# Kernel tuning notes

Hardware: AMD Instinct MI355X
Metric: run time of the kernel (lower is better)

## Reference

```python
import jax, jax.numpy as jnp
import numpy as np

B, T, E = 2, 2048, 1024
H, D = 8, 512
ROPE_BASE = 10000.0


def apply_rope(x):
    # x: [B, H, T, D] -- rotary positional embedding, half-split convention
    t = x.shape[2]
    d = x.shape[3]
    inv_freq = 1.0 / (ROPE_BASE ** (jnp.arange(0, d, 2, dtype=jnp.float32) / d))  # [D/2]
    ang = jnp.arange(t, dtype=jnp.float32)[:, None] * inv_freq[None, :]           # [T, D/2]
    cos = jnp.cos(ang)[None, None].astype(x.dtype)
    sin = jnp.sin(ang)[None, None].astype(x.dtype)
    x1, x2 = jnp.split(x, 2, axis=-1)
    return jnp.concatenate([x1 * cos - x2 * sin, x1 * sin + x2 * cos], axis=-1)


def setup_inputs() -> dict:
    key = jax.random.key(0)
    ks = jax.random.split(key, 5)
    s_in = 1.0 / np.sqrt(E)
    s_out = 1.0 / np.sqrt(H * D)
    return {
        "x": jax.random.normal(ks[0], (B, T, E), dtype=jnp.float32),
        "Wq": jax.random.normal(ks[1], (H * D, E), dtype=jnp.float32) * s_in,
        "Wk": jax.random.normal(ks[2], (H * D, E), dtype=jnp.float32) * s_in,
        "Wv": jax.random.normal(ks[3], (H * D, E), dtype=jnp.float32) * s_in,
        "Wo": jax.random.normal(ks[4], (E, H * D), dtype=jnp.float32) * s_out,
    }


def reference(x, Wq, Wk, Wv, Wo):
    b, t, e = x.shape
    # QKV projections (bias-free Linear: x @ W.T), reshape to [B, H, T, D]
    q = (x @ Wq.T).reshape(b, t, H, D).transpose(0, 2, 1, 3)
    k = (x @ Wk.T).reshape(b, t, H, D).transpose(0, 2, 1, 3)
    v = (x @ Wv.T).reshape(b, t, H, D).transpose(0, 2, 1, 3)
    # RoPE on q and k
    q = apply_rope(q)
    k = apply_rope(k)
    # scaled dot-product attention with causal mask
    scale = 1.0 / jnp.sqrt(jnp.asarray(D, dtype=x.dtype))
    scores = jnp.einsum("bhqd,bhkd->bhqk", q, k) * scale
    causal = jnp.tril(jnp.ones((t, t), dtype=bool))
    scores = jnp.where(causal[None, None], scores, jnp.asarray(-jnp.inf, dtype=scores.dtype))
    probs = jax.nn.softmax(scores, axis=-1)  # explicitly materialized, as in source
    attn = jnp.einsum("bhqk,bhkd->bhqd", probs, v)
    out = attn.transpose(0, 2, 1, 3).reshape(b, t, H * D) @ Wo.T
    return out
```

## Files before the change

### kernel.cpp

```cpp
#include <hip/hip_runtime.h>


#define DEV __device__ __forceinline__

using bf16x8  = __attribute__((ext_vector_type(8))) short;
using floatx4 = __attribute__((ext_vector_type(4))) float;

#define MFMA16(a, b, c) __builtin_amdgcn_mfma_f32_16x16x32_bf16((a), (b), (c), 0, 0, 0)

#define KT_BH 1097728
#define KT_TILE 17152
#define KT_ROW 536
#define VT_BH 1310720
#define VT_TILE 20480

DEV unsigned short f2bf(float f) {
  union { float f; unsigned int u; } c; c.f = f;
  unsigned int u = c.u + 0x7FFFu + ((c.u >> 16) & 1u);
  return (unsigned short)(u >> 16);
}
DEV float bf2f(unsigned short h) {
  union { unsigned int u; float f; } c; c.u = ((unsigned int)h) << 16;
  return c.f;
}

DEV void ldsld16(const unsigned short* g, unsigned short* l) {
  __builtin_amdgcn_global_load_lds(
      (__attribute__((address_space(1))) void*)(g),
      (__attribute__((address_space(3))) void*)(l), 16, 0, 0);
}

__global__ void cast4_k(const float* __restrict__ x,  const float* __restrict__ wq,
                        const float* __restrict__ wk, const float* __restrict__ wv,
                        unsigned short* __restrict__ xb,  unsigned short* __restrict__ wqb,
                        unsigned short* __restrict__ wkb, unsigned short* __restrict__ wvb) {
  const float* s; unsigned short* d;
  switch (blockIdx.y) {
    case 0: s = x;  d = xb;  break;
    case 1: s = wq; d = wqb; break;
    case 2: s = wk; d = wkb; break;
    default: s = wv; d = wvb; break;
  }
  int i = blockIdx.x * 256 + threadIdx.x;
  float4 v = ((const float4*)s)[i];
  uint2 o;
  o.x = (unsigned int)f2bf(v.x) | ((unsigned int)f2bf(v.y) << 16);
  o.y = (unsigned int)f2bf(v.z) | ((unsigned int)f2bf(v.w) << 16);
  ((uint2*)d)[i] = o;
}

__global__ void cast1_k(const float* __restrict__ s, unsigned short* __restrict__ d) {
  int i = blockIdx.x * 256 + threadIdx.x;
  float4 v = ((const float4*)s)[i];
  uint2 o;
  o.x = (unsigned int)f2bf(v.x) | ((unsigned int)f2bf(v.y) << 16);
  o.y = (unsigned int)f2bf(v.z) | ((unsigned int)f2bf(v.w) << 16);
  ((uint2*)d)[i] = o;
}

__global__ __launch_bounds__(256) void qkv_gemm(
    const unsigned short* __restrict__ X,
    const unsigned short* __restrict__ Wq, const unsigned short* __restrict__ Wk,
    const unsigned short* __restrict__ Wv,
    unsigned short* __restrict__ Qo, unsigned short* __restrict__ Ko, unsigned short* __restrict__ Vo) {
  __shared__ __align__(16) unsigned short As[128 * 32];
  __shared__ __align__(16) unsigned short Bs[128 * 32];
  const int tid = threadIdx.x;
  const int wave = tid >> 6, lane = tid & 63, quad = lane >> 4, l16 = lane & 15;
  const int m0 = blockIdx.x * 128, n0 = blockIdx.y * 128;
  const int z = blockIdx.z;
  const unsigned short* W = (z == 0) ? Wq : (z == 1) ? Wk : Wv;
  const int wm = (wave >> 1) * 64, wn = (wave & 1) * 64;
  floatx4 acc[4][4];
#pragma unroll
  for (int i = 0; i < 4; ++i)
#pragma unroll
    for (int j = 0; j < 4; ++j) acc[i][j] = (floatx4){0.f, 0.f, 0.f, 0.f};

  const int r0 = wave * 32;
  const int lrow = lane >> 2, lchunk = (lane & 3) * 8;
  for (int k0 = 0; k0 < 1024; k0 += 32) {
    const unsigned short* ga = X + (size_t)(m0 + r0 + lrow) * 1024 + k0 + lchunk;
    const unsigned short* gb = W + (size_t)(n0 + r0 + lrow) * 1024 + k0 + lchunk;
    ldsld16(ga, As + r0 * 32);
    ldsld16(ga + (size_t)16 * 1024, As + r0 * 32 + 512);
    ldsld16(gb, Bs + r0 * 32);
    ldsld16(gb + (size_t)16 * 1024, Bs + r0 * 32 + 512);
    __syncthreads();
    bf16x8 af[4], bw[4];
#pragma unroll
    for (int i = 0; i < 4; ++i) af[i] = *(const bf16x8*)(As + (wm + i * 16 + l16) * 32 + quad * 8);
#pragma unroll
    for (int j = 0; j < 4; ++j) bw[j] = *(const bf16x8*)(Bs + (wn + j * 16 + l16) * 32 + quad * 8);
#pragma unroll
    for (int i = 0; i < 4; ++i)
#pragma unroll
      for (int j = 0; j < 4; ++j) acc[i][j] = MFMA16(af[i], bw[j], acc[i][j]);
    __syncthreads();
  }
#pragma unroll
  for (int i = 0; i < 4; ++i)
#pragma unroll
    for (int j = 0; j < 4; ++j) {
      int gn = n0 + wn + j * 16 + l16;
      int h = gn >> 9, d = gn & 511;
      int gm0 = m0 + wm + i * 16 + quad * 4;
      int b = gm0 >> 11, t0 = gm0 & 2047;
      int bh = b * 8 + h;
      if (z == 2) {
        unsigned short pk[4];
#pragma unroll
        for (int r = 0; r < 4; ++r) pk[r] = f2bf(acc[i][j][r]);
        size_t off = (size_t)bh * VT_BH + (t0 >> 5) * VT_TILE + (size_t)d * 40 + (t0 & 31);
        *(uint2*)(Vo + off) = *(uint2*)pk;
      } else if (z == 1) {
        size_t off = (size_t)bh * KT_BH + (t0 >> 5) * KT_TILE + (size_t)(t0 & 31) * KT_ROW + d;
#pragma unroll
        for (int r = 0; r < 4; ++r) Ko[off + (size_t)r * KT_ROW] = f2bf(acc[i][j][r]);
      } else {
        size_t base = ((size_t)(bh * 2048 + t0)) * 512 + d;
#pragma unroll
        for (int r = 0; r < 4; ++r) Qo[base + (size_t)r * 512] = f2bf(acc[i][j][r]);
      }
    }
}

__global__ void rope_k(unsigned short* __restrict__ Q, unsigned short* __restrict__ Kt) {
  int idx = blockIdx.x * 256 + threadIdx.x;
  int r = idx & 8388607;
  int row = r >> 8;
  int i = r & 255;
  int t = row & 2047;
  unsigned short* P;
  size_t base;
  if (idx & 8388608) {
    int bh = row >> 11;
    base = (size_t)bh * KT_BH + (t >> 5) * KT_TILE + (size_t)(t & 31) * KT_ROW;
    P = Kt;
  } else {
    base = (size_t)row * 512;
    P = Q;
  }
  float x1 = bf2f(P[base + i]);
  float x2 = bf2f(P[base + i + 256]);
  float freq = expf(-(float)i * 0.03597789207803197f);
  float ang = (float)t * freq;
  float sv, cv;
  sincosf(ang, &sv, &cv);
  P[base + i]       = f2bf(x1 * cv - x2 * sv);
  P[base + i + 256] = f2bf(x1 * sv + x2 * cv);
}

__global__ __launch_bounds__(512, 2) void flash_attn(
    const unsigned short* __restrict__ Q, const unsigned short* __restrict__ Kt,
    const unsigned short* __restrict__ Vt, unsigned short* __restrict__ attn,
    unsigned short* __restrict__ P1, float* __restrict__ ml1, float* __restrict__ ml2,
    int split) {
  __shared__ __align__(16) unsigned short Ks[2 * 32 * 536];
  __shared__ __align__(16) unsigned short Vs[2 * 512 * 40];
  __shared__ __align__(16) unsigned short Ps[8 * 16 * 40];
  const int tid = threadIdx.x;
  const int wave = tid >> 6, lane = tid & 63, quad = lane >> 4, l16 = lane & 15;
  const int bh = blockIdx.x, b = bh >> 3, head = bh & 7;
  const int y = blockIdx.y;
  int qi, st0 = 0, stN, om = 0;
  if (split) {
    if (y == 0)      { qi = 9; stN = 4 * qi + 4; }
    else if (y == 1) { qi = 8; stN = 4 * qi + 4; }
    else if (y < 14) {
      qi = 15 - ((y - 2) >> 1);
      int mid = 2 * qi + 2;
      if ((y & 1) == 0) { st0 = 0;   stN = mid;        om = 1; }
      else              { st0 = mid; stN = 4 * qi + 4; om = 2; }
    } else { qi = 7 - (y - 14); stN = 4 * qi + 4; }
  } else { qi = 15 - y; stN = 4 * qi + 4; }

  const unsigned short* Qp = Q + ((size_t)bh << 20);
  const unsigned short* Kp = Kt + (size_t)bh * KT_BH;
  const unsigned short* Vp = Vt + (size_t)bh * VT_BH;
  const int qb = qi * 128;
  const int qw0 = qb + wave * 16;

  bf16x8 qf[16];
  {
    const unsigned short* qrow = Qp + (size_t)(qw0 + l16) * 512 + quad * 8;
#pragma unroll
    for (int ks = 0; ks < 16; ++ks) qf[ks] = *(const bf16x8*)(qrow + ks * 32);
  }
  floatx4 o[32];
#pragma unroll
  for (int n = 0; n < 32; ++n) o[n] = (floatx4){0.f, 0.f, 0.f, 0.f};
  float m_[4], l_[4];
#pragma unroll
  for (int r = 0; r < 4; ++r) { m_[r] = -3.0e38f; l_[r] = 0.f; }

  unsigned short* psw = Ps + wave * 640;
  const int kc0 = wave * 268;
  const int vc0 = wave * 320;

  {
    const unsigned short* gk = Kp + (size_t)st0 * KT_TILE;
    const unsigned short* gv = Vp + (size_t)st0 * VT_TILE;
#pragma unroll
    for (int j = 0; j < 4; ++j)
      ldsld16(gk + (size_t)(kc0 + j * 64 + lane) * 8, Ks + (kc0 + j * 64) * 8);
    if (lane < 12) ldsld16(gk + (size_t)(kc0 + 256 + lane) * 8, Ks + (kc0 + 256) * 8);
#pragma unroll
    for (int j = 0; j < 5; ++j)
      ldsld16(gv + (size_t)(vc0 + j * 64 + lane) * 8, Vs + (vc0 + j * 64) * 8);
  }

  for (int st = st0; st < stN; ++st) {
    const int cur = (st - st0) & 1;
    __syncthreads();
    if (st + 1 < stN) {
      const int nxt = cur ^ 1;
      const unsigned short* gk = Kp + (size_t)(st + 1) * KT_TILE;
      const unsigned short* gv = Vp + (size_t)(st + 1) * VT_TILE;
      unsigned short* kd = Ks + nxt * 17152;
      unsigned short* vd = Vs + nxt * 20480;
#pragma unroll
      for (int j = 0; j < 4; ++j)
        ldsld16(gk + (size_t)(kc0 + j * 64 + lane) * 8, kd + (kc0 + j * 64) * 8);
      if (lane < 12) ldsld16(gk + (size_t)(kc0 + 256 + lane) * 8, kd + (kc0 + 256) * 8);
#pragma unroll
      for (int j = 0; j < 5; ++j)
        ldsld16(gv + (size_t)(vc0 + j * 64 + lane) * 8, vd + (vc0 + j * 64) * 8);
    }
    const unsigned short* ksb = Ks + cur * 17152;
    const unsigned short* vsb = Vs + cur * 20480;
    const int s0 = st * 32;
    floatx4 sc0 = (floatx4){0.f, 0.f, 0.f, 0.f}, sc1 = sc0;
#pragma unroll
    for (int ks = 0; ks < 16; ++ks) {
      bf16x8 k0 = *(const bf16x8*)(ksb + (size_t)l16 * 536 + ks * 32 + quad * 8);
      bf16x8 k1 = *(const bf16x8*)(ksb + (size_t)(16 + l16) * 536 + ks * 32 + quad * 8);
      sc0 = MFMA16(qf[ks], k0, sc0);
      sc1 = MFMA16(qf[ks], k1, sc1);
    }
    const float scale = 0.04419417382415922f;
    const int qrow0 = qw0 + quad * 4;
    float pv0[4], pv1[4], mr[4];
#pragma unroll
    for (int r = 0; r < 4; ++r) {
      float a0 = sc0[r] * scale, a1 = sc1[r] * scale;
      if (s0 + l16 > qrow0 + r) a0 = -3.0e38f;
      if (s0 + 16 + l16 > qrow0 + r) a1 = -3.0e38f;
      pv0[r] = a0; pv1[r] = a1;
      mr[r] = fmaxf(a0, a1);
    }
#pragma unroll
    for (int off = 1; off < 16; off <<= 1)
#pragma unroll
      for (int r = 0; r < 4; ++r) mr[r] = fmaxf(mr[r], __shfl_xor(mr[r], off, 64));
    float alpha[4], rs[4];
#pragma unroll
    for (int r = 0; r < 4; ++r) {
      float mn = fmaxf(m_[r], mr[r]);
      alpha[r] = __expf(m_[r] - mn);
      m_[r] = mn;
      float p0 = __expf(pv0[r] - mn);
      float p1 = __expf(pv1[r] - mn);
      rs[r] = p0 + p1;
      psw[(quad * 4 + r) * 40 + l16] = f2bf(p0);
      psw[(quad * 4 + r) * 40 + 16 + l16] = f2bf(p1);
    }
#pragma unroll
    for (int off = 1; off < 16; off <<= 1)
#pragma unroll
      for (int r = 0; r < 4; ++r) rs[r] += __shfl_xor(rs[r], off, 64);
#pragma unroll
    for (int r = 0; r < 4; ++r) l_[r] = l_[r] * alpha[r] + rs[r];
    if (__any(alpha[0] + alpha[1] + alpha[2] + alpha[3] < 4.0f)) {
#pragma unroll
      for (int n = 0; n < 32; ++n)
#pragma unroll
        for (int r = 0; r < 4; ++r) o[n][r] *= alpha[r];
    }
    bf16x8 pf = *(const bf16x8*)(psw + (size_t)l16 * 40 + quad * 8);
#pragma unroll
    for (int nt = 0; nt < 32; ++nt) {
      bf16x8 vf = *(const bf16x8*)(vsb + (size_t)(nt * 16 + l16) * 40 + quad * 8);
      o[nt] = MFMA16(pf, vf, o[nt]);
    }
  }
  const int rowi = wave * 16 + quad * 4;
  if (om == 0) {
    float inv[4];
#pragma unroll
    for (int r = 0; r < 4; ++r) inv[r] = 1.0f / l_[r];
    unsigned short* arow = attn + ((size_t)(b * 2048 + qb + rowi)) * 4096 + head * 512 + l16;
#pragma unroll
    for (int nt = 0; nt < 32; ++nt)
#pragma unroll
      for (int r = 0; r < 4; ++r)
        arow[(size_t)r * 4096 + nt * 16] = f2bf(o[nt][r] * inv[r]);
  } else {
    const int p = bh * 6 + (qi - 10);
    float* ml = (om == 1) ? ml1 : ml2;
    if (l16 == 0) {
#pragma unroll
      for (int r = 0; r < 4; ++r) {
        ml[(size_t)p * 256 + (rowi + r) * 2]     = m_[r];
        ml[(size_t)p * 256 + (rowi + r) * 2 + 1] = l_[r];
      }
    }
    if (om == 1) {
      unsigned short* prow = P1 + ((size_t)p * 128 + rowi) * 512 + l16;
#pragma unroll
      for (int nt = 0; nt < 32; ++nt)
#pragma unroll
        for (int r = 0; r < 4; ++r)
          prow[(size_t)r * 512 + nt * 16] = f2bf(o[nt][r]);
    } else {
      unsigned short* arow = attn + ((size_t)(b * 2048 + qb + rowi)) * 4096 + head * 512 + l16;
#pragma unroll
      for (int nt = 0; nt < 32; ++nt)
#pragma unroll
        for (int r = 0; r < 4; ++r)
          arow[(size_t)r * 4096 + nt * 16] = f2bf(o[nt][r]);
    }
  }
}

__global__ void combine_k(const unsigned short* __restrict__ P1,
                          const float* __restrict__ ml1, const float* __restrict__ ml2,
                          unsigned short* __restrict__ attn) {
  const int p = blockIdx.x;
  const int bh = p / 6, qi = 10 + (p - bh * 6);
  const int b = bh >> 3, head = bh & 7;
  const int tid = threadIdx.x;
#pragma unroll
  for (int it = 0; it < 32; ++it) {
    int idx = it * 256 + tid;
    int row = idx >> 6, c8 = (idx & 63) * 8;
    float m1 = ml1[(size_t)p * 256 + row * 2], l1 = ml1[(size_t)p * 256 + row * 2 + 1];
    float m2 = ml2[(size_t)p * 256 + row * 2], l2 = ml2[(size_t)p * 256 + row * 2 + 1];
    float M = fmaxf(m1, m2);
    float w1 = __expf(m1 - M), w2 = __expf(m2 - M);
    float inv = 1.0f / (l1 * w1 + l2 * w2);
    const unsigned short* o1 = P1 + ((size_t)p * 128 + row) * 512 + c8;
    unsigned short* ap = attn + ((size_t)(b * 2048 + qi * 128 + row)) * 4096 + head * 512 + c8;
    unsigned short res[8];
#pragma unroll
    for (int j = 0; j < 8; ++j)
      res[j] = f2bf((bf2f(o1[j]) * w1 + bf2f(ap[j]) * w2) * inv);
    *(bf16x8*)ap = *(bf16x8*)res;
  }
}

__global__ __launch_bounds__(256) void out_gemm(
    const unsigned short* __restrict__ A, const unsigned short* __restrict__ W,
    float* __restrict__ C) {
  __shared__ __align__(16) unsigned short As[128 * 32];
  __shared__ __align__(16) unsigned short Bs[128 * 32];
  const int tid = threadIdx.x;
  const int wave = tid >> 6, lane = tid & 63, quad = lane >> 4, l16 = lane & 15;
  const int m0 = blockIdx.x * 128, n0 = blockIdx.y * 128;
  const int kb = blockIdx.z * 1024;
  const int wm = (wave >> 1) * 64, wn = (wave & 1) * 64;
  floatx4 acc[4][4];
#pragma unroll
  for (int i = 0; i < 4; ++i)
#pragma unroll
    for (int j = 0; j < 4; ++j) acc[i][j] = (floatx4){0.f, 0.f, 0.f, 0.f};
  const int r0 = wave * 32;
  const int lrow = lane >> 2, lchunk = (lane & 3) * 8;
  for (int k0 = kb; k0 < kb + 1024; k0 += 32) {
    const unsigned short* ga = A + (size_t)(m0 + r0 + lrow) * 4096 + k0 + lchunk;
    const unsigned short* gb = W + (size_t)(n0 + r0 + lrow) * 4096 + k0 + lchunk;
    ldsld16(ga, As + r0 * 32);
    ldsld16(ga + (size_t)16 * 4096, As + r0 * 32 + 512);
    ldsld16(gb, Bs + r0 * 32);
    ldsld16(gb + (size_t)16 * 4096, Bs + r0 * 32 + 512);
    __syncthreads();
    bf16x8 af[4], bw[4];
#pragma unroll
    for (int i = 0; i < 4; ++i) af[i] = *(const bf16x8*)(As + (wm + i * 16 + l16) * 32 + quad * 8);
#pragma unroll
    for (int j = 0; j < 4; ++j) bw[j] = *(const bf16x8*)(Bs + (wn + j * 16 + l16) * 32 + quad * 8);
#pragma unroll
    for (int i = 0; i < 4; ++i)
#pragma unroll
      for (int j = 0; j < 4; ++j) acc[i][j] = MFMA16(af[i], bw[j], acc[i][j]);
    __syncthreads();
  }
#pragma unroll
  for (int i = 0; i < 4; ++i)
#pragma unroll
    for (int j = 0; j < 4; ++j) {
      int gn = n0 + wn + j * 16 + l16;
#pragma unroll
      for (int r = 0; r < 4; ++r) {
        int gm = m0 + wm + i * 16 + quad * 4 + r;
        unsafeAtomicAdd(&C[(size_t)gm * 1024 + gn], acc[i][j][r]);
      }
    }
}

extern "C" void kernel_launch(void* const* d_in, const int* in_sizes, int n_in,
                              void* d_out, int out_size, void* d_ws, size_t ws_size,
                              hipStream_t stream) {
  const float* x  = (const float*)d_in[0];
  const float* Wq = (const float*)d_in[1];
  const float* Wk = (const float*)d_in[2];
  const float* Wv = (const float*)d_in[3];
  const float* Wo = (const float*)d_in[4];
  float* out = (float*)d_out;
  char* ws = (char*)d_ws;
  const size_t MB = 1048576;
  unsigned short* xb    = (unsigned short*)(ws + 0 * MB);
  unsigned short* wqb   = (unsigned short*)(ws + 8 * MB);
  unsigned short* wkb   = (unsigned short*)(ws + 16 * MB);
  unsigned short* wvb   = (unsigned short*)(ws + 24 * MB);
  unsigned short* attnb = (unsigned short*)(ws + 0 * MB);
  unsigned short* Qb    = (unsigned short*)(ws + 32 * MB);
  unsigned short* wob   = (unsigned short*)(ws + 32 * MB);
  unsigned short* Ktb   = (unsigned short*)(ws + 64 * MB);
  unsigned short* Vtb   = (unsigned short*)(ws + 98 * MB);
  unsigned short* P1    = (unsigned short*)(ws + 138 * MB);
  float* ml1            = (float*)(ws + 154 * MB);
  float* ml2            = (float*)(ws + 154 * MB + 131072);
  const int split = (ws_size >= (size_t)160 * MB) ? 1 : 0;

  hipMemsetAsync(d_out, 0, (size_t)4096 * 1024 * 4, stream);

  cast4_k<<<dim3(4096, 4), 256, 0, stream>>>(x, Wq, Wk, Wv, xb, wqb, wkb, wvb);
  qkv_gemm<<<dim3(32, 32, 3), 256, 0, stream>>>(xb, wqb, wkb, wvb, Qb, Ktb, Vtb);
  rope_k<<<65536, 256, 0, stream>>>(Qb, Ktb);
  flash_attn<<<dim3(16, split ? 22 : 16), 512, 0, stream>>>(Qb, Ktb, Vtb, attnb, P1, ml1, ml2, split);
  if (split) combine_k<<<96, 256, 0, stream>>>(P1, ml1, ml2, attnb);
  cast1_k<<<4096, 256, 0, stream>>>(Wo, wob);
  out_gemm<<<dim3(32, 8, 4), 256, 0, stream>>>(attnb, wob, out);
}
```

Measured before the change: 613.2 us.

## Switch flash attention to 32x32 MFMA with 4 waves and rebalanced split

The attention kernel now uses 4 waves of 32 query rows each with 32x32x16 bf16 MFMA in place of 8 waves with 16x16 tiles. It keeps a single running max per wave, computes row sums with an MFMA against a ones vector, and skips the causal mask on tiles that are fully visible. The split schedule now covers 8 query blocks (24 y-blocks) via lookup tables, with the combine grid grown to match. The aim is to raise MFMA throughput and cut shuffle reductions, at the cost of heavy register pressure (16 floatx16 accumulators plus 32 Q fragments) and the loss of per-row max precision.

```diff
diff --git a/kernel.cpp b/kernel.cpp
--- a/kernel.cpp
+++ b/kernel.cpp
@@ -3,10 +3,12 @@
 
 #define DEV __device__ __forceinline__
 
-using bf16x8  = __attribute__((ext_vector_type(8))) short;
-using floatx4 = __attribute__((ext_vector_type(4))) float;
+using bf16x8   = __attribute__((ext_vector_type(8))) short;
+using floatx4  = __attribute__((ext_vector_type(4))) float;
+using floatx16 = __attribute__((ext_vector_type(16))) float;
 
 #define MFMA16(a, b, c) __builtin_amdgcn_mfma_f32_16x16x32_bf16((a), (b), (c), 0, 0, 0)
+#define MFMA32(a, b, c) __builtin_amdgcn_mfma_f32_32x32x16_bf16((a), (b), (c), 0, 0, 0)
 
 #define KT_BH 1097728
 #define KT_TILE 17152
@@ -151,62 +153,70 @@
   P[base + i + 256] = f2bf(x1 * sv + x2 * cv);
 }
 
-__global__ __launch_bounds__(512, 2) void flash_attn(
+static __device__ const signed char JQI[24] = {15,15,7,14,14,13,13,6,12,12,11,11,5,10,10,9,9,4,8,8,3,2,1,0};
+static __device__ const signed char JCH[24] = {0,1,-1,0,1,0,1,-1,0,1,0,1,-1,0,1,0,1,-1,0,1,-1,-1,-1,-1};
+
+__global__ __launch_bounds__(256, 1) void flash_attn(
     const unsigned short* __restrict__ Q, const unsigned short* __restrict__ Kt,
     const unsigned short* __restrict__ Vt, unsigned short* __restrict__ attn,
     unsigned short* __restrict__ P1, float* __restrict__ ml1, float* __restrict__ ml2,
     int split) {
-  __shared__ __align__(16) unsigned short Ks[2 * 32 * 536];
-  __shared__ __align__(16) unsigned short Vs[2 * 512 * 40];
-  __shared__ __align__(16) unsigned short Ps[8 * 16 * 40];
+  __shared__ __align__(16) unsigned short Ks[2 * 17152];
+  __shared__ __align__(16) unsigned short Vs[2 * 20480];
+  __shared__ __align__(16) unsigned short Ps[4 * 1280];
   const int tid = threadIdx.x;
-  const int wave = tid >> 6, lane = tid & 63, quad = lane >> 4, l16 = lane & 15;
+  const int wave = tid >> 6, lane = tid & 63;
+  const int col = lane & 31, half = lane >> 5;
   const int bh = blockIdx.x, b = bh >> 3, head = bh & 7;
   const int y = blockIdx.y;
-  int qi, st0 = 0, stN, om = 0;
+  int qi, st0, stN, om;
   if (split) {
-    if (y == 0)      { qi = 9; stN = 4 * qi + 4; }
-    else if (y == 1) { qi = 8; stN = 4 * qi + 4; }
-    else if (y < 14) {
-      qi = 15 - ((y - 2) >> 1);
-      int mid = 2 * qi + 2;
-      if ((y & 1) == 0) { st0 = 0;   stN = mid;        om = 1; }
-      else              { st0 = mid; stN = 4 * qi + 4; om = 2; }
-    } else { qi = 7 - (y - 14); stN = 4 * qi + 4; }
-  } else { qi = 15 - y; stN = 4 * qi + 4; }
+    qi = JQI[y];
+    int ch = JCH[y];
+    if (ch < 0)       { st0 = 0;          stN = 4 * qi + 4; om = 0; }
+    else if (ch == 0) { st0 = 0;          stN = 2 * qi + 2; om = 1; }
+    else              { st0 = 2 * qi + 2; stN = 4 * qi + 4; om = 2; }
+  } else { qi = 15 - y; st0 = 0; stN = 4 * qi + 4; om = 0; }
 
   const unsigned short* Qp = Q + ((size_t)bh << 20);
   const unsigned short* Kp = Kt + (size_t)bh * KT_BH;
   const unsigned short* Vp = Vt + (size_t)bh * VT_BH;
   const int qb = qi * 128;
-  const int qw0 = qb + wave * 16;
-
-  bf16x8 qf[16];
+  const int qw0 = qb + wave * 32;
+
+  bf16x8 qf[32];
   {
-    const unsigned short* qrow = Qp + (size_t)(qw0 + l16) * 512 + quad * 8;
-#pragma unroll
-    for (int ks = 0; ks < 16; ++ks) qf[ks] = *(const bf16x8*)(qrow + ks * 32);
-  }
-  floatx4 o[32];
-#pragma unroll
-  for (int n = 0; n < 32; ++n) o[n] = (floatx4){0.f, 0.f, 0.f, 0.f};
-  float m_[4], l_[4];
-#pragma unroll
-  for (int r = 0; r < 4; ++r) { m_[r] = -3.0e38f; l_[r] = 0.f; }
-
-  unsigned short* psw = Ps + wave * 640;
-  const int kc0 = wave * 268;
-  const int vc0 = wave * 320;
+    const unsigned short* qrow = Qp + (size_t)(qw0 + col) * 512 + half * 8;
+#pragma unroll
+    for (int ks = 0; ks < 32; ++ks) qf[ks] = *(const bf16x8*)(qrow + ks * 16);
+  }
+  floatx16 o[16];
+#pragma unroll
+  for (int n = 0; n < 16; ++n)
+#pragma unroll
+    for (int r = 0; r < 16; ++r) o[n][r] = 0.f;
+  float l_[16];
+#pragma unroll
+  for (int r = 0; r < 16; ++r) l_[r] = 0.f;
+  float m_ = -3.0e38f;
+
+  bf16x8 ones;
+#pragma unroll
+  for (int j = 0; j < 8; ++j) ones[j] = (short)0x3F80;
+
+  unsigned short* psw = Ps + wave * 1280;
+  const int kc0 = wave * 536;
+  const int vc0 = wave * 640;
 
   {
     const unsigned short* gk = Kp + (size_t)st0 * KT_TILE;
     const unsigned short* gv = Vp + (size_t)st0 * VT_TILE;
 #pragma unroll
-    for (int j = 0; j < 4; ++j)
+    for (int j = 0; j < 8; ++j)
       ldsld16(gk + (size_t)(kc0 + j * 64 + lane) * 8, Ks + (kc0 + j * 64) * 8);
-    if (lane < 12) ldsld16(gk + (size_t)(kc0 + 256 + lane) * 8, Ks + (kc0 + 256) * 8);
-#pragma unroll
-    for (int j = 0; j < 5; ++j)
+    if (lane < 24) ldsld16(gk + (size_t)(kc0 + 512 + lane) * 8, Ks + (kc0 + 512) * 8);
+#pragma unroll
+    for (int j = 0; j < 10; ++j)
       ldsld16(gv + (size_t)(vc0 + j * 64 + lane) * 8, Vs + (vc0 + j * 64) * 8);
   }
 
@@ -220,105 +230,115 @@
       unsigned short* kd = Ks + nxt * 17152;
       unsigned short* vd = Vs + nxt * 20480;
 #pragma unroll
-      for (int j = 0; j < 4; ++j)
+      for (int j = 0; j < 8; ++j)
         ldsld16(gk + (size_t)(kc0 + j * 64 + lane) * 8, kd + (kc0 + j * 64) * 8);
-      if (lane < 12) ldsld16(gk + (size_t)(kc0 + 256 + lane) * 8, kd + (kc0 + 256) * 8);
-#pragma unroll
-      for (int j = 0; j < 5; ++j)
+      if (lane < 24) ldsld16(gk + (size_t)(kc0 + 512 + lane) * 8, kd + (kc0 + 512) * 8);
+#pragma unroll
+      for (int j = 0; j < 10; ++j)
         ldsld16(gv + (size_t)(vc0 + j * 64 + lane) * 8, vd + (vc0 + j * 64) * 8);
     }
     const unsigned short* ksb = Ks + cur * 17152;
     const unsigned short* vsb = Vs + cur * 20480;
     const int s0 = st * 32;
-    floatx4 sc0 = (floatx4){0.f, 0.f, 0.f, 0.f}, sc1 = sc0;
-#pragma unroll
-    for (int ks = 0; ks < 16; ++ks) {
-      bf16x8 k0 = *(const bf16x8*)(ksb + (size_t)l16 * 536 + ks * 32 + quad * 8);
-      bf16x8 k1 = *(const bf16x8*)(ksb + (size_t)(16 + l16) * 536 + ks * 32 + quad * 8);
-      sc0 = MFMA16(qf[ks], k0, sc0);
-      sc1 = MFMA16(qf[ks], k1, sc1);
+    floatx16 s;
+#pragma unroll
+    for (int r = 0; r < 16; ++r) s[r] = 0.f;
+    {
+      const unsigned short* kr = ksb + (size_t)col * KT_ROW + half * 8;
+#pragma unroll
+      for (int ks = 0; ks < 32; ++ks) {
+        bf16x8 kf = *(const bf16x8*)(kr + ks * 16);
+        s = MFMA32(qf[ks], kf, s);
+      }
     }
     const float scale = 0.04419417382415922f;
-    const int qrow0 = qw0 + quad * 4;
-    float pv0[4], pv1[4], mr[4];
-#pragma unroll
-    for (int r = 0; r < 4; ++r) {
-      float a0 = sc0[r] * scale, a1 = sc1[r] * scale;
-      if (s0 + l16 > qrow0 + r) a0 = -3.0e38f;
-      if (s0 + 16 + l16 > qrow0 + r) a1 = -3.0e38f;
-      pv0[r] = a0; pv1[r] = a1;
-      mr[r] = fmaxf(a0, a1);
-    }
-#pragma unroll
-    for (int off = 1; off < 16; off <<= 1)
-#pragma unroll
-      for (int r = 0; r < 4; ++r) mr[r] = fmaxf(mr[r], __shfl_xor(mr[r], off, 64));
-    float alpha[4], rs[4];
-#pragma unroll
-    for (int r = 0; r < 4; ++r) {
-      float mn = fmaxf(m_[r], mr[r]);
-      alpha[r] = __expf(m_[r] - mn);
-      m_[r] = mn;
-      float p0 = __expf(pv0[r] - mn);
-      float p1 = __expf(pv1[r] - mn);
-      rs[r] = p0 + p1;
-      psw[(quad * 4 + r) * 40 + l16] = f2bf(p0);
-      psw[(quad * 4 + r) * 40 + 16 + l16] = f2bf(p1);
-    }
-#pragma unroll
-    for (int off = 1; off < 16; off <<= 1)
-#pragma unroll
-      for (int r = 0; r < 4; ++r) rs[r] += __shfl_xor(rs[r], off, 64);
-#pragma unroll
-    for (int r = 0; r < 4; ++r) l_[r] = l_[r] * alpha[r] + rs[r];
-    if (__any(alpha[0] + alpha[1] + alpha[2] + alpha[3] < 4.0f)) {
-#pragma unroll
-      for (int n = 0; n < 32; ++n)
-#pragma unroll
-        for (int r = 0; r < 4; ++r) o[n][r] *= alpha[r];
-    }
-    bf16x8 pf = *(const bf16x8*)(psw + (size_t)l16 * 40 + quad * 8);
-#pragma unroll
-    for (int nt = 0; nt < 32; ++nt) {
-      bf16x8 vf = *(const bf16x8*)(vsb + (size_t)(nt * 16 + l16) * 40 + quad * 8);
-      o[nt] = MFMA16(pf, vf, o[nt]);
-    }
-  }
-  const int rowi = wave * 16 + quad * 4;
+    const bool need_mask = (s0 + 31 > qw0);
+    float mt = -3.0e38f;
+#pragma unroll
+    for (int r = 0; r < 16; ++r) {
+      float a = s[r] * scale;
+      if (need_mask) {
+        int qrow = qw0 + (r & 3) + 8 * (r >> 2) + 4 * half;
+        if (s0 + col > qrow) a = -3.0e38f;
+      }
+      s[r] = a;
+      mt = fmaxf(mt, a);
+    }
+#pragma unroll
+    for (int off = 1; off < 64; off <<= 1) mt = fmaxf(mt, __shfl_xor(mt, off, 64));
+    float mn = fmaxf(m_, mt);
+    float alpha = __expf(m_ - mn);
+    m_ = mn;
+    {
+      unsigned short* pw = psw + (4 * half) * 40 + col;
+#pragma unroll
+      for (int r = 0; r < 16; ++r) {
+        float p = __expf(s[r] - m_);
+        pw[((r & 3) + 8 * (r >> 2)) * 40] = f2bf(p);
+      }
+    }
+    bf16x8 pf0 = *(const bf16x8*)(psw + (size_t)col * 40 + half * 8);
+    bf16x8 pf1 = *(const bf16x8*)(psw + (size_t)col * 40 + 16 + half * 8);
+    floatx16 ls;
+#pragma unroll
+    for (int r = 0; r < 16; ++r) ls[r] = 0.f;
+    ls = MFMA32(pf0, ones, ls);
+    ls = MFMA32(pf1, ones, ls);
+    if (alpha < 1.0f) {
+#pragma unroll
+      for (int n = 0; n < 16; ++n)
+#pragma unroll
+        for (int r = 0; r < 16; ++r) o[n][r] *= alpha;
+#pragma unroll
+      for (int r = 0; r < 16; ++r) l_[r] *= alpha;
+    }
+#pragma unroll
+    for (int r = 0; r < 16; ++r) l_[r] += ls[r];
+#pragma unroll
+    for (int nt = 0; nt < 16; ++nt) {
+      const unsigned short* vr = vsb + (size_t)(nt * 32 + col) * 40 + half * 8;
+      bf16x8 v0 = *(const bf16x8*)(vr);
+      bf16x8 v1 = *(const bf16x8*)(vr + 16);
+      o[nt] = MFMA32(pf0, v0, o[nt]);
+      o[nt] = MFMA32(pf1, v1, o[nt]);
+    }
+  }
+  const int rb = wave * 32 + 4 * half;
   if (om == 0) {
-    float inv[4];
-#pragma unroll
-    for (int r = 0; r < 4; ++r) inv[r] = 1.0f / l_[r];
-    unsigned short* arow = attn + ((size_t)(b * 2048 + qb + rowi)) * 4096 + head * 512 + l16;
-#pragma unroll
-    for (int nt = 0; nt < 32; ++nt)
-#pragma unroll
-      for (int r = 0; r < 4; ++r)
-        arow[(size_t)r * 4096 + nt * 16] = f2bf(o[nt][r] * inv[r]);
+    float inv[16];
+#pragma unroll
+    for (int r = 0; r < 16; ++r) inv[r] = 1.0f / l_[r];
+    unsigned short* arow = attn + ((size_t)(b * 2048 + qb + rb)) * 4096 + head * 512 + col;
+#pragma unroll
+    for (int nt = 0; nt < 16; ++nt)
+#pragma unroll
+      for (int r = 0; r < 16; ++r)
+        arow[(size_t)((r & 3) + 8 * (r >> 2)) * 4096 + nt * 32] = f2bf(o[nt][r] * inv[r]);
   } else {
-    const int p = bh * 6 + (qi - 10);
+    const int p = bh * 8 + (qi - 8);
     float* ml = (om == 1) ? ml1 : ml2;
-    if (l16 == 0) {
-#pragma unroll
-      for (int r = 0; r < 4; ++r) {
-        ml[(size_t)p * 256 + (rowi + r) * 2]     = m_[r];
-        ml[(size_t)p * 256 + (rowi + r) * 2 + 1] = l_[r];
+    if (col == 0) {
+#pragma unroll
+      for (int r = 0; r < 16; ++r) {
+        int row = rb + (r & 3) + 8 * (r >> 2);
+        ml[(size_t)p * 256 + row * 2]     = m_;
+        ml[(size_t)p * 256 + row * 2 + 1] = l_[r];
       }
     }
     if (om == 1) {
-      unsigned short* prow = P1 + ((size_t)p * 128 + rowi) * 512 + l16;
-#pragma unroll
-      for (int nt = 0; nt < 32; ++nt)
-#pragma unroll
-        for (int r = 0; r < 4; ++r)
-          prow[(size_t)r * 512 + nt * 16] = f2bf(o[nt][r]);
+      unsigned short* prow = P1 + ((size_t)p * 128 + rb) * 512 + col;
+#pragma unroll
+      for (int nt = 0; nt < 16; ++nt)
+#pragma unroll
+        for (int r = 0; r < 16; ++r)
+          prow[(size_t)((r & 3) + 8 * (r >> 2)) * 512 + nt * 32] = f2bf(o[nt][r]);
     } else {
-      unsigned short* arow = attn + ((size_t)(b * 2048 + qb + rowi)) * 4096 + head * 512 + l16;
-#pragma unroll
-      for (int nt = 0; nt < 32; ++nt)
-#pragma unroll
-        for (int r = 0; r < 4; ++r)
-          arow[(size_t)r * 4096 + nt * 16] = f2bf(o[nt][r]);
+      unsigned short* arow = attn + ((size_t)(b * 2048 + qb + rb)) * 4096 + head * 512 + col;
+#pragma unroll
+      for (int nt = 0; nt < 16; ++nt)
+#pragma unroll
+        for (int r = 0; r < 16; ++r)
+          arow[(size_t)((r & 3) + 8 * (r >> 2)) * 4096 + nt * 32] = f2bf(o[nt][r]);
     }
   }
 }
@@ -327,7 +347,7 @@
                           const float* __restrict__ ml1, const float* __restrict__ ml2,
                           unsigned short* __restrict__ attn) {
   const int p = blockIdx.x;
-  const int bh = p / 6, qi = 10 + (p - bh * 6);
+  const int bh = p >> 3, qi = 8 + (p & 7);
   const int b = bh >> 3, head = bh & 7;
   const int tid = threadIdx.x;
 #pragma unroll
@@ -428,8 +448,8 @@
   cast4_k<<<dim3(4096, 4), 256, 0, stream>>>(x, Wq, Wk, Wv, xb, wqb, wkb, wvb);
   qkv_gemm<<<dim3(32, 32, 3), 256, 0, stream>>>(xb, wqb, wkb, wvb, Qb, Ktb, Vtb);
   rope_k<<<65536, 256, 0, stream>>>(Qb, Ktb);
-  flash_attn<<<dim3(16, split ? 22 : 16), 512, 0, stream>>>(Qb, Ktb, Vtb, attnb, P1, ml1, ml2, split);
-  if (split) combine_k<<<96, 256, 0, stream>>>(P1, ml1, ml2, attnb);
+  flash_attn<<<dim3(16, split ? 24 : 16), 256, 0, stream>>>(Qb, Ktb, Vtb, attnb, P1, ml1, ml2, split);
+  if (split) combine_k<<<128, 256, 0, stream>>>(P1, ml1, ml2, attnb);
   cast1_k<<<4096, 256, 0, stream>>>(Wo, wob);
   out_gemm<<<dim3(32, 8, 4), 256, 0, stream>>>(attnb, wob, out);
 }
```

Result: slower. 1.430 ms (+133.2%).
